# Kernel optimization log

Measured on AMD Instinct MI355X. Metric: run time of the kernel, lower is better.

Reference implementation:

```python
import jax, jax.numpy as jnp
import numpy as np

N, D, F, H, DH, R = 50000, 16, 256, 8, 32, 20
HOP_NUM, TOP_K, ALPHA, NEG_SLOPE = 10, 5, 0.1, 0.2
FF_HID = 4 * F


def _ln(x, g, b, eps=1e-5):
    m = x.mean(-1, keepdims=True)
    v = ((x - m) ** 2).mean(-1, keepdims=True)
    return (x - m) / jnp.sqrt(v + eps) * g + b


def setup_inputs() -> dict:
    key = jax.random.key(0)
    ks = jax.random.split(key, 16)
    s = 0.02
    inp = {
        'ent_feat': jax.random.normal(ks[0], (N, F), jnp.float32),
        'rel_feat': jax.random.normal(ks[1], (R, F), jnp.float32),
        'W_head': jax.random.normal(ks[2], (F, H * DH), jnp.float32) * s,
        'W_tail': jax.random.normal(ks[3], (F, H * DH), jnp.float32) * s,
        'W_ent': jax.random.normal(ks[4], (F, H * DH), jnp.float32) * s,
        'W_rel': jax.random.normal(ks[5], (F, H * DH), jnp.float32) * s,
        'attn_h': jax.random.normal(ks[6], (H, DH), jnp.float32) * s,
        'attn_t': jax.random.normal(ks[7], (H, DH), jnp.float32) * s,
        'attn_r': jax.random.normal(ks[8], (H, DH), jnp.float32) * s,
        'ln_ent_g': jnp.ones((F,), jnp.float32), 'ln_ent_b': jnp.zeros((F,), jnp.float32),
        'ln_rel_g': jnp.ones((F,), jnp.float32), 'ln_rel_b': jnp.zeros((F,), jnp.float32),
        'ln_ff_g': jnp.ones((F,), jnp.float32), 'ln_ff_b': jnp.zeros((F,), jnp.float32),
        'ffn_W1': jax.random.normal(ks[9], (F, FF_HID), jnp.float32) * s,
        'ffn_b1': jnp.zeros((FF_HID,), jnp.float32),
        'ffn_W2': jax.random.normal(ks[10], (FF_HID, F), jnp.float32) * s,
        'ffn_b2': jnp.zeros((F,), jnp.float32),
        'src': jax.random.randint(ks[11], (N, D), 0, N, jnp.int32),
        'rid': jax.random.randint(ks[12], (N, D), 0, R, jnp.int32),
    }
    return inp


def reference(ent_feat, rel_feat, W_head, W_tail, W_ent, W_rel,
              attn_h, attn_t, attn_r,
              ln_ent_g, ln_ent_b, ln_rel_g, ln_rel_b, ln_ff_g, ln_ff_b,
              ffn_W1, ffn_b1, ffn_W2, ffn_b2, src, rid):
    # --- projections (dropout = 0 at eval) ---
    x = _ln(ent_feat, ln_ent_g, ln_ent_b)                    # [N,F]
    fh = (x @ W_head).reshape(N, H, DH)
    ftl = (x @ W_tail).reshape(N, H, DH)
    fe = (x @ W_ent).reshape(N, H, DH)                       # 'ft' messages
    r = _ln(rel_feat, ln_rel_g, ln_rel_b)
    fr = (r @ W_rel).reshape(R, H, DH)
    # --- per-node / per-relation attention logits ---
    eh = (fh * attn_h).sum(-1)                               # [N,H]
    et = (ftl * attn_t).sum(-1)                              # [N,H]
    er = (fr * attn_r).sum(-1)                               # [R,H]
    # edges: row i = incoming edges of dst node i, sources src[i,:]
    e = eh[src] + et[:, None, :] + er[rid]                   # [N,D,H]
    e = jnp.where(e > 0, e, NEG_SLOPE * e)                   # LeakyReLU
    # --- edge_softmax over incoming edges of each dst node ---
    a = jax.nn.softmax(e, axis=1)                            # [N,D,H]
    # --- top-k sparsification + renormalization ---
    a_t = a.transpose(0, 2, 1)                               # [N,H,D]
    topv, _ = jax.lax.top_k(a_t, TOP_K)                      # [N,H,K]
    kth = topv[..., TOP_K - 1]                               # [N,H]
    top_sum = topv.sum(-1)                                   # [N,H]
    a_n = jnp.where(a_t >= kth[..., None], a_t, 0.0) / top_sum[..., None]  # [N,H,D]
    # --- PPR diffusion: feat <- (1-a) * A @ feat + a * feat0 ---
    feat0 = fe

    def step(feat, _):
        m = feat[src]                                        # [N,D,H,DH]
        agg = jnp.einsum('ndhk,nhd->nhk', m, a_n)            # [N,H,DH]
        return (1.0 - ALPHA) * agg + ALPHA * feat0, None

    feat, _ = jax.lax.scan(step, feat0, None, length=HOP_NUM)
    # --- residual (Identity since in==out) + FFN block ---
    rst = feat + ent_feat.reshape(N, H, DH)
    rst = rst.reshape(N, F)
    y = _ln(rst, ln_ff_g, ln_ff_b)
    ff = jax.nn.relu(y @ ffn_W1 + ffn_b1) @ ffn_W2 + ffn_b2
    return ff + rst
```

## Files before the change

### kernel.cpp

```cpp
#include <hip/hip_runtime.h>

#define NN   50000
#define DD   16
#define FFE  256
#define HH   8
#define DHH  32
#define RR   20
#define HOPN 10

typedef unsigned short u16;
typedef unsigned int   u32;
typedef __attribute__((ext_vector_type(8))) short  short8;
typedef __attribute__((ext_vector_type(4))) float  floatx4;
typedef __attribute__((ext_vector_type(4))) double doublex4;

__device__ __forceinline__ float b2f(u16 u){ return __uint_as_float(((u32)u)<<16); }
__device__ __forceinline__ u16 f2b(float f){
  u32 x = __float_as_uint(f);
  u32 r = (x + 0x7fffu + ((x>>16)&1u)) >> 16;
  return (u16)r;
}

__device__ __forceinline__ void glds16(const u16* g, u16* l) {
  __builtin_amdgcn_global_load_lds(
      (const __attribute__((address_space(1))) void*)g,
      (__attribute__((address_space(3))) void*)l, 16, 0, 0);
}

__global__ __launch_bounds__(256) void castw_kernel(
    const float* __restrict__ We, const float* __restrict__ W1,
    const float* __restrict__ W2,
    u16* __restrict__ Wet, u16* __restrict__ W1t, u16* __restrict__ W2t)
{
  int tid = blockIdx.x*256 + threadIdx.x;
  if (tid < 256*256) {
    int k = tid >> 8, n = tid & 255;
    Wet[n*256 + k] = f2b(We[tid]);
  } else if (tid < 256*256 + 256*1024) {
    int s = tid - 65536;
    int k = s >> 10, n = s & 1023;
    W1t[n*256 + k] = f2b(W1[s]);
  } else if (tid < 589824) {
    int s = tid - 327680;
    int k = s >> 8, n = s & 255;
    W2t[n*1024 + k] = f2b(W2[s]);
  }
}

__global__ __launch_bounds__(256) void prep_kernel(
    const float* __restrict__ rel_feat,
    const float* __restrict__ W_head, const float* __restrict__ W_tail,
    const float* __restrict__ W_rel,
    const float* __restrict__ attn_h, const float* __restrict__ attn_t,
    const float* __restrict__ attn_r,
    const float* __restrict__ lng, const float* __restrict__ lnb,
    double* __restrict__ Wcomb, double* __restrict__ er)
{
  int t = threadIdx.x;
  if (blockIdx.x == RR) {
    for (int h = 0; h < HH; h++) {
      double sh = 0.0, st = 0.0;
      #pragma unroll
      for (int c = 0; c < DHH; c++) {
        int j = h*DHH + c;
        sh += (double)W_head[t*FFE + j] * (double)attn_h[j];
        st += (double)W_tail[t*FFE + j] * (double)attn_t[j];
      }
      Wcomb[t*16 + h]     = sh;
      Wcomb[t*16 + 8 + h] = st;
    }
    return;
  }
  int r = blockIdx.x;
  __shared__ double red[8];
  __shared__ double rln[256];
  double v = (double)rel_feat[r*FFE + t];
  double s = v, q = v*v;
  #pragma unroll
  for (int o = 32; o; o >>= 1) { s += __shfl_xor(s, o, 64); q += __shfl_xor(q, o, 64); }
  if ((t & 63) == 0) { red[t>>6] = s; red[4 + (t>>6)] = q; }
  __syncthreads();
  double stot = red[0]+red[1]+red[2]+red[3];
  double qtot = red[4]+red[5]+red[6]+red[7];
  double mean = stot * (1.0/256.0);
  double var  = qtot * (1.0/256.0) - mean*mean;
  double rstd = 1.0 / sqrt(var + 1e-5);
  rln[t] = (v - mean) * rstd * (double)lng[t] + (double)lnb[t];
  __syncthreads();
  double acc = 0.0;
  for (int k = 0; k < 256; k++) acc += rln[k] * (double)W_rel[k*FFE + t];
  double p = acc * (double)attn_r[t];
  #pragma unroll
  for (int o = 16; o; o >>= 1) p += __shfl_down(p, o, 32);
  if ((t & 31) == 0) er[r*HH + (t>>5)] = p;
}

__global__ __launch_bounds__(256) void logits_kernel(
    const float* __restrict__ ent,
    const float* __restrict__ lng, const float* __restrict__ lnb,
    const double* __restrict__ Wcomb,
    u16* __restrict__ xb, double* __restrict__ eh, double* __restrict__ et)
{
  __shared__ double xs[16][257];
  int tid = threadIdx.x;
  int i0 = blockIdx.x * 16;
  int wave = tid >> 6, lane = tid & 63;
  for (int m = wave; m < 16; m += 4) {
    int row = i0 + m;
    float4 u = *(const float4*)&ent[row*FFE + lane*4];
    double v0 = u.x, v1 = u.y, v2 = u.z, v3 = u.w;
    double s = v0+v1+v2+v3;
    double q = v0*v0 + v1*v1 + v2*v2 + v3*v3;
    #pragma unroll
    for (int o = 32; o; o >>= 1) { s += __shfl_xor(s, o, 64); q += __shfl_xor(q, o, 64); }
    double mean = s * (1.0/256.0);
    double var  = q * (1.0/256.0) - mean*mean;
    double rstd = 1.0 / sqrt(var + 1e-5);
    float4 ug = *(const float4*)&lng[lane*4];
    float4 ub = *(const float4*)&lnb[lane*4];
    double y0 = (v0-mean)*rstd*(double)ug.x + (double)ub.x;
    double y1 = (v1-mean)*rstd*(double)ug.y + (double)ub.y;
    double y2 = (v2-mean)*rstd*(double)ug.z + (double)ub.z;
    double y3 = (v3-mean)*rstd*(double)ug.w + (double)ub.w;
    int c = lane*4;
    xs[m][c] = y0; xs[m][c+1] = y1; xs[m][c+2] = y2; xs[m][c+3] = y3;
    ushort4 o4;
    o4.x = f2b((float)y0); o4.y = f2b((float)y1);
    o4.z = f2b((float)y2); o4.w = f2b((float)y3);
    *(ushort4*)&xb[row*FFE + c] = o4;
  }
  __syncthreads();
  int nl = lane & 15, kg = lane >> 4;
  doublex4 c4 = {0.0, 0.0, 0.0, 0.0};
  #pragma unroll
  for (int kk = 0; kk < 16; kk++) {
    int k = wave*64 + kk*4 + kg;
    double a = xs[nl][k];
    double b = Wcomb[k*16 + nl];
    c4 = __builtin_amdgcn_mfma_f64_16x16x4f64(a, b, c4, 0, 0, 0);
  }
  __syncthreads();
  double* sp = &xs[0][0];
  #pragma unroll
  for (int i = 0; i < 4; i++)
    sp[wave*256 + (kg*4 + i)*16 + nl] = c4[i];
  __syncthreads();
  int m = tid >> 4, n = tid & 15;
  double v = sp[tid] + sp[256 + tid] + sp[512 + tid] + sp[768 + tid];
  if (n < 8) eh[(i0+m)*HH + n] = v;
  else       et[(i0+m)*HH + (n-8)] = v;
}

template<int EPI>
__global__ __launch_bounds__(256) void gemm_kernel(
    const u16* __restrict__ A, const u16* __restrict__ B,
    const float* __restrict__ bias,
    const u16* __restrict__ feat, const float* __restrict__ ent,
    u16* __restrict__ Obf, float* __restrict__ Of,
    int M, int N, int K)
{
  __shared__ u16 As[128*64];
  __shared__ u16 Bs[128*64];
  int t = threadIdx.x;
  int i0 = blockIdx.x * 128;
  int n0 = blockIdx.y * 128;
  int w = t >> 6, l = t & 63;
  int wr = w >> 1, wc = w & 1;

  int lrow = l >> 3;
  int scol = ((l & 7) ^ lrow) * 8;

  int ln = l & 15, q = l >> 4;
  int colk0 = (q*8) ^ ((ln & 7) << 3);
  int colk1 = colk0 ^ 32;

  floatx4 acc[4][4];
  #pragma unroll
  for (int mt = 0; mt < 4; mt++)
    #pragma unroll
    for (int nt = 0; nt < 4; nt++) acc[mt][nt] = (floatx4){0.f,0.f,0.f,0.f};

  for (int k0 = 0; k0 < K; k0 += 64) {
    #pragma unroll
    for (int j = 0; j < 4; j++) {
      int ra = w*32 + j*8 + lrow;
      int ga = min(i0 + ra, M-1);
      glds16(&A[(size_t)ga*K + k0 + scol], &As[(w*4+j)*512]);
      int gb = n0 + ra;
      glds16(&B[(size_t)gb*K + k0 + scol], &Bs[(w*4+j)*512]);
    }
    __syncthreads();
    #pragma unroll
    for (int ks = 0; ks < 2; ks++) {
      int ck = ks ? colk1 : colk0;
      short8 bfr[4], afr[4];
      #pragma unroll
      for (int nt = 0; nt < 4; nt++)
        bfr[nt] = *(const short8*)&Bs[(wc*64 + nt*16 + ln)*64 + ck];
      #pragma unroll
      for (int mt = 0; mt < 4; mt++)
        afr[mt] = *(const short8*)&As[(wr*64 + mt*16 + ln)*64 + ck];
      #pragma unroll
      for (int mt = 0; mt < 4; mt++)
        #pragma unroll
        for (int nt = 0; nt < 4; nt++)
          acc[mt][nt] = __builtin_amdgcn_mfma_f32_16x16x32_bf16(afr[mt], bfr[nt], acc[mt][nt], 0, 0, 0);
    }
    __syncthreads();
  }

  int lr = q * 4;
  #pragma unroll
  for (int mt = 0; mt < 4; mt++) {
    #pragma unroll
    for (int nt = 0; nt < 4; nt++) {
      int col = n0 + wc*64 + nt*16 + ln;
      #pragma unroll
      for (int r = 0; r < 4; r++) {
        int row = i0 + wr*64 + mt*16 + lr + r;
        if (row < M) {
          float v = acc[mt][nt][r];
          if (EPI == 0) {
            Obf[(size_t)row*N + col] = f2b(v);
          } else if (EPI == 1) {
            v += bias[col];
            Obf[(size_t)row*N + col] = f2b(v > 0.f ? v : 0.f);
          } else {
            v += bias[col] + b2f(feat[(size_t)row*FFE + col]) + ent[(size_t)row*FFE + col];
            Of[(size_t)row*N + col] = v;
          }
        }
      }
    }
  }
}

__global__ __launch_bounds__(256) void edge_kernel(
    const int* __restrict__ src, const int* __restrict__ rid,
    const double* __restrict__ eh, const double* __restrict__ et,
    const double* __restrict__ er,
    int* __restrict__ idx6, float* __restrict__ w6)
{
  int tid = blockIdx.x*256 + threadIdx.x;
  if (tid >= NN*HH) return;
  int i = tid >> 3, h = tid & 7;
  double bet = et[tid];
  double e[16]; int sj[16];
  #pragma unroll
  for (int d = 0; d < 16; d++) {
    int s = src[i*DD + d];
    int rv = rid[i*DD + d];
    sj[d] = s;
    double v = eh[s*HH + h] + bet + er[rv*HH + h];
    e[d] = (v > 0.0) ? v : 0.2 * v;
  }
  u32 mask = 0; double vs[5]; int js[5];
  #pragma unroll
  for (int k = 0; k < 5; k++) {
    double best = -1e300; int bj = 0, bd = 0;
    #pragma unroll
    for (int d = 0; d < 16; d++) {
      bool c = (((mask>>d)&1u) == 0u) && (e[d] > best);
      if (c) { best = e[d]; bj = sj[d]; bd = d; }
    }
    mask |= (1u << bd); vs[k] = best; js[k] = bj;
  }
  double kth = vs[4];
  int j6 = 0; bool f6 = false;
  #pragma unroll
  for (int d = 0; d < 16; d++) {
    if ((((mask>>d)&1u) == 0u) && (e[d] == kth) && !f6) { j6 = sj[d]; f6 = true; }
  }
  float m0 = (float)vs[0];
  float ex[5], ssum = 0.f;
  #pragma unroll
  for (int k = 0; k < 5; k++) { ex[k] = __expf((float)vs[k] - m0); ssum += ex[k]; }
  float inv = 0.9f / ssum;
  long base = (long)tid * 6;
  #pragma unroll
  for (int k = 0; k < 5; k++) { idx6[base+k] = js[k]; w6[base+k] = ex[k]*inv; }
  idx6[base+5] = j6; w6[base+5] = f6 ? ex[4]*inv : 0.f;
}

__global__ __launch_bounds__(256) void diff_kernel(
    const u16* __restrict__ fold, const u16* __restrict__ fe,
    const int* __restrict__ idx6, const float* __restrict__ w6,
    u16* __restrict__ fnew)
{
  int tid = threadIdx.x;
  int nb = tid >> 5;
  int v  = tid & 31;
  int h  = v >> 2;
  int cc = (v & 3) * 8;
  int i  = blockIdx.x*8 + nb;
  int ch = h*DHH + cc;
  long eb = ((long)i*HH + h) * 6;

  int jj[5]; float wv[5];
  #pragma unroll
  for (int k = 0; k < 5; k++) { jj[k] = idx6[eb + k]; wv[k] = w6[eb + k]; }
  short8 g[5];
  #pragma unroll
  for (int k = 0; k < 5; k++)
    g[k] = *(const short8*)&fold[(size_t)jj[k]*FFE + ch];
  short8 f8 = *(const short8*)&fe[(size_t)i*FFE + ch];

  float acc[8];
  #pragma unroll
  for (int j = 0; j < 8; j++) acc[j] = 0.1f * b2f((u16)f8[j]);
  #pragma unroll
  for (int k = 0; k < 5; k++)
    #pragma unroll
    for (int j = 0; j < 8; j++) acc[j] += wv[k] * b2f((u16)g[k][j]);

  float w5 = w6[eb + 5];
  if (w5 != 0.f) {
    int j5 = idx6[eb + 5];
    short8 g5 = *(const short8*)&fold[(size_t)j5*FFE + ch];
    #pragma unroll
    for (int j = 0; j < 8; j++) acc[j] += w5 * b2f((u16)g5[j]);
  }

  short8 o8;
  #pragma unroll
  for (int j = 0; j < 8; j++) o8[j] = (short)f2b(acc[j]);
  *(short8*)&fnew[(size_t)i*FFE + ch] = o8;
}

__global__ __launch_bounds__(256) void ln_ff_kernel(
    const u16* __restrict__ feat, const float* __restrict__ ent,
    const float* __restrict__ g, const float* __restrict__ b,
    u16* __restrict__ y)
{
  int w = threadIdx.x >> 6, l = threadIdx.x & 63;
  int row = blockIdx.x*4 + w;
  float4 e4 = *(const float4*)&ent[row*FFE + l*4];
  ushort4 fv = *(const ushort4*)&feat[row*FFE + l*4];
  float v0 = b2f(fv.x)+e4.x, v1 = b2f(fv.y)+e4.y;
  float v2 = b2f(fv.z)+e4.z, v3 = b2f(fv.w)+e4.w;
  float s = v0+v1+v2+v3;
  float q = v0*v0 + v1*v1 + v2*v2 + v3*v3;
  #pragma unroll
  for (int o = 32; o; o >>= 1) { s += __shfl_xor(s, o, 64); q += __shfl_xor(q, o, 64); }
  float mean = s * (1.f/256.f);
  float var  = q * (1.f/256.f) - mean*mean;
  float rstd = rsqrtf(var + 1e-5f);
  float4 g4 = *(const float4*)&g[l*4];
  float4 b4 = *(const float4*)&b[l*4];
  ushort4 o4;
  o4.x = f2b((v0-mean)*rstd*g4.x + b4.x);
  o4.y = f2b((v1-mean)*rstd*g4.y + b4.y);
  o4.z = f2b((v2-mean)*rstd*g4.z + b4.z);
  o4.w = f2b((v3-mean)*rstd*g4.w + b4.w);
  *(ushort4*)&y[row*FFE + l*4] = o4;
}

extern "C" void kernel_launch(void* const* d_in, const int* in_sizes, int n_in,
                              void* d_out, int out_size, void* d_ws, size_t ws_size,
                              hipStream_t stream)
{
  const float* ent      = (const float*)d_in[0];
  const float* rel      = (const float*)d_in[1];
  const float* W_head   = (const float*)d_in[2];
  const float* W_tail   = (const float*)d_in[3];
  const float* W_ent    = (const float*)d_in[4];
  const float* W_rel    = (const float*)d_in[5];
  const float* attn_h   = (const float*)d_in[6];
  const float* attn_t   = (const float*)d_in[7];
  const float* attn_r   = (const float*)d_in[8];
  const float* ln_ent_g = (const float*)d_in[9];
  const float* ln_ent_b = (const float*)d_in[10];
  const float* ln_rel_g = (const float*)d_in[11];
  const float* ln_rel_b = (const float*)d_in[12];
  const float* ln_ff_g  = (const float*)d_in[13];
  const float* ln_ff_b  = (const float*)d_in[14];
  const float* W1       = (const float*)d_in[15];
  const float* b1       = (const float*)d_in[16];
  const float* W2       = (const float*)d_in[17];
  const float* b2       = (const float*)d_in[18];
  const int* src        = (const int*)d_in[19];
  const int* rid        = (const int*)d_in[20];
  float* out = (float*)d_out;

  char* w = (char*)d_ws;
  double* er64  = (double*)(w + 0);
  double* Wcomb = (double*)(w + 4096);
  double* eh64 = (double*)(w + 36864);
  double* et64 = (double*)(w + 3236864);
  u16*    xb   = (u16*)  (w + 6436864);
  u16*    fe   = (u16*)  (w + 32036864);
  u16*    fA   = (u16*)  (w + 57636864);
  int*    idx6 = (int*)  (w + 83236864);
  float*  w6   = (float*)(w + 92836864);
  u16*    h1   = (u16*)  (w + 0);
  u16*    fB   = (u16*)  (w + 102436864);
  u16*    y    = (u16*)  (w + 128036864);
  u16*    Wet  = (u16*)  (w + 153636864);
  u16*    W1t  = (u16*)  (w + 153767936);
  u16*    W2t  = (u16*)  (w + 154292224);

  castw_kernel<<<2304, 256, 0, stream>>>(W_ent, W1, W2, Wet, W1t, W2t);
  prep_kernel<<<RR+1, 256, 0, stream>>>(rel, W_head, W_tail, W_rel,
                                        attn_h, attn_t, attn_r,
                                        ln_rel_g, ln_rel_b, Wcomb, er64);
  logits_kernel<<<NN/16, 256, 0, stream>>>(ent, ln_ent_g, ln_ent_b, Wcomb,
                                           xb, eh64, et64);
  {
    dim3 g((NN + 127)/128, 2);
    gemm_kernel<0><<<g, 256, 0, stream>>>(xb, Wet, nullptr, nullptr, nullptr,
                                          fe, nullptr, NN, 256, 256);
  }
  edge_kernel<<<(NN*HH + 255)/256, 256, 0, stream>>>(src, rid, eh64, et64, er64,
                                                     idx6, w6);
  const u16* cur = fe;
  u16* bufs[2] = { fA, fB };
  for (int hop = 0; hop < HOPN; hop++) {
    u16* nxt = bufs[hop & 1];
    diff_kernel<<<NN/8, 256, 0, stream>>>(cur, fe, idx6, w6, nxt);
    cur = nxt;
  }
  ln_ff_kernel<<<NN/4, 256, 0, stream>>>(cur, ent, ln_ff_g, ln_ff_b, y);
  {
    dim3 g((NN + 127)/128, 8);
    gemm_kernel<1><<<g, 256, 0, stream>>>(y, W1t, b1, nullptr, nullptr,
                                          h1, nullptr, NN, 1024, 256);
  }
  {
    dim3 g((NN + 127)/128, 2);
    gemm_kernel<2><<<g, 256, 0, stream>>>(h1, W2t, b2, cur, ent,
                                          nullptr, out, NN, 256, 1024);
  }
}
```

Baseline: 776.6 us.

## Fuse FFN GEMMs into one kernel and pack edge indices with weights

Replaces the two FFN GEMM launches with a single kernel that keeps the 64x1024 hidden activation in shared memory chunk by chunk, so the N×1024 bf16 intermediate is never written to or read back from global memory. The edge kernel now stores indices and weights interleaved in one 12-int record, so the diffusion kernel reads them with three vector loads instead of twelve scalar loads. In exchange, the fused kernel reads W1/W2 fragments straight from global memory without LDS staging, and it runs with small tiles and fewer blocks, which may reduce MFMA efficiency.

```diff
diff --git a/kernel.cpp b/kernel.cpp
--- a/kernel.cpp
+++ b/kernel.cpp
@@ -166,10 +166,8 @@
   int n0 = blockIdx.y * 128;
   int w = t >> 6, l = t & 63;
   int wr = w >> 1, wc = w & 1;
-
   int lrow = l >> 3;
   int scol = ((l & 7) ^ lrow) * 8;
-
   int ln = l & 15, q = l >> 4;
   int colk0 = (q*8) ^ ((ln & 7) << 3);
   int colk1 = colk0 ^ 32;
@@ -235,11 +233,120 @@
   }
 }
 
+__global__ __launch_bounds__(256) void ffn_kernel(
+    const u16* __restrict__ y, const u16* __restrict__ W1t,
+    const float* __restrict__ b1, const u16* __restrict__ W2t,
+    const float* __restrict__ b2, const u16* __restrict__ feat,
+    const float* __restrict__ ent, float* __restrict__ out, int M)
+{
+  __shared__ u16 ys[64*256];
+  __shared__ u16 hs[64*128];
+  int t = threadIdx.x;
+  int w = t >> 6, l = t & 63;
+  int i0 = blockIdx.x * 64;
+  int ln = l & 15, q = l >> 4;
+
+  {
+    int rsub = l >> 5;
+    int gsub = l & 31;
+    #pragma unroll
+    for (int j = 0; j < 8; j++) {
+      int r = w*16 + j*2 + rsub;
+      int gr = min(i0 + r, M-1);
+      int so = (gsub ^ ((j*2 + rsub) & 7)) * 8;
+      glds16(&y[(size_t)gr*FFE + so], &ys[(w*16 + j*2)*FFE]);
+    }
+  }
+  __syncthreads();
+
+  floatx4 acc2[4][4];
+  #pragma unroll
+  for (int mt = 0; mt < 4; mt++)
+    #pragma unroll
+    for (int nt = 0; nt < 4; nt++) acc2[mt][nt] = (floatx4){0.f,0.f,0.f,0.f};
+
+  for (int s = 0; s < 8; s++) {
+    floatx4 acc1[4][2];
+    #pragma unroll
+    for (int mt = 0; mt < 4; mt++)
+      #pragma unroll
+      for (int nt = 0; nt < 2; nt++) acc1[mt][nt] = (floatx4){0.f,0.f,0.f,0.f};
+    #pragma unroll
+    for (int ks = 0; ks < 8; ks++) {
+      short8 bf[2];
+      #pragma unroll
+      for (int nt = 0; nt < 2; nt++) {
+        int n = s*128 + w*32 + nt*16 + ln;
+        bf[nt] = *(const short8*)&W1t[(size_t)n*FFE + ks*32 + q*8];
+      }
+      int gsw = ((ks*4 + q) ^ (ln & 7)) * 8;
+      #pragma unroll
+      for (int mt = 0; mt < 4; mt++) {
+        short8 af = *(const short8*)&ys[(mt*16 + ln)*FFE + gsw];
+        #pragma unroll
+        for (int nt = 0; nt < 2; nt++)
+          acc1[mt][nt] = __builtin_amdgcn_mfma_f32_16x16x32_bf16(af, bf[nt], acc1[mt][nt], 0, 0, 0);
+      }
+    }
+    #pragma unroll
+    for (int mt = 0; mt < 4; mt++) {
+      #pragma unroll
+      for (int nt = 0; nt < 2; nt++) {
+        int hid = w*32 + nt*16 + ln;
+        float bb = b1[s*128 + hid];
+        #pragma unroll
+        for (int r = 0; r < 4; r++) {
+          int row = mt*16 + q*4 + r;
+          float v = acc1[mt][nt][r] + bb;
+          int gs = (hid >> 3) ^ (row & 7);
+          hs[row*128 + gs*8 + (hid & 7)] = f2b(v > 0.f ? v : 0.f);
+        }
+      }
+    }
+    __syncthreads();
+    #pragma unroll
+    for (int ks = 0; ks < 4; ks++) {
+      short8 bf[4];
+      #pragma unroll
+      for (int nt = 0; nt < 4; nt++) {
+        int n = w*64 + nt*16 + ln;
+        bf[nt] = *(const short8*)&W2t[(size_t)n*1024 + s*128 + ks*32 + q*8];
+      }
+      int gsw = ((ks*4 + q) ^ (ln & 7)) * 8;
+      #pragma unroll
+      for (int mt = 0; mt < 4; mt++) {
+        short8 af = *(const short8*)&hs[(mt*16 + ln)*128 + gsw];
+        #pragma unroll
+        for (int nt = 0; nt < 4; nt++)
+          acc2[mt][nt] = __builtin_amdgcn_mfma_f32_16x16x32_bf16(af, bf[nt], acc2[mt][nt], 0, 0, 0);
+      }
+    }
+    __syncthreads();
+  }
+
+  #pragma unroll
+  for (int mt = 0; mt < 4; mt++) {
+    #pragma unroll
+    for (int nt = 0; nt < 4; nt++) {
+      int col = w*64 + nt*16 + ln;
+      #pragma unroll
+      for (int r = 0; r < 4; r++) {
+        int row = i0 + mt*16 + q*4 + r;
+        if (row < M) {
+          float v = acc2[mt][nt][r];
+          v += b2[col] + b2f(feat[(size_t)row*FFE + col]) + ent[(size_t)row*FFE + col];
+          out[(size_t)row*FFE + col] = v;
+        }
+      }
+    }
+  }
+}
+
 __global__ __launch_bounds__(256) void edge_kernel(
     const int* __restrict__ src, const int* __restrict__ rid,
     const double* __restrict__ eh, const double* __restrict__ et,
     const double* __restrict__ er,
-    int* __restrict__ idx6, float* __restrict__ w6)
+    int* __restrict__ pk)
 {
   int tid = blockIdx.x*256 + threadIdx.x;
   if (tid >= NN*HH) return;
@@ -276,15 +383,19 @@
   #pragma unroll
   for (int k = 0; k < 5; k++) { ex[k] = __expf((float)vs[k] - m0); ssum += ex[k]; }
   float inv = 0.9f / ssum;
-  long base = (long)tid * 6;
-  #pragma unroll
-  for (int k = 0; k < 5; k++) { idx6[base+k] = js[k]; w6[base+k] = ex[k]*inv; }
-  idx6[base+5] = j6; w6[base+5] = f6 ? ex[4]*inv : 0.f;
+  long base = (long)tid * 12;
+  #pragma unroll
+  for (int k = 0; k < 5; k++) {
+    pk[base + k]     = js[k];
+    pk[base + 6 + k] = __float_as_int(ex[k]*inv);
+  }
+  pk[base + 5]  = j6;
+  pk[base + 11] = __float_as_int(f6 ? ex[4]*inv : 0.f);
 }
 
 __global__ __launch_bounds__(256) void diff_kernel(
     const u16* __restrict__ fold, const u16* __restrict__ fe,
-    const int* __restrict__ idx6, const float* __restrict__ w6,
+    const int* __restrict__ pk,
     u16* __restrict__ fnew)
 {
   int tid = threadIdx.x;
@@ -294,11 +405,16 @@
   int cc = (v & 3) * 8;
   int i  = blockIdx.x*8 + nb;
   int ch = h*DHH + cc;
-  long eb = ((long)i*HH + h) * 6;
-
-  int jj[5]; float wv[5];
-  #pragma unroll
-  for (int k = 0; k < 5; k++) { jj[k] = idx6[eb + k]; wv[k] = w6[eb + k]; }
+  long base = ((long)i*HH + h) * 12;
+
+  int4 pa = *(const int4*)&pk[base];
+  int4 pb = *(const int4*)&pk[base + 4];
+  int4 pc = *(const int4*)&pk[base + 8];
+  int jj[5] = { pa.x, pa.y, pa.z, pa.w, pb.x };
+  float wv[5] = { __int_as_float(pb.z), __int_as_float(pb.w),
+                  __int_as_float(pc.x), __int_as_float(pc.y),
+                  __int_as_float(pc.z) };
+
   short8 g[5];
   #pragma unroll
   for (int k = 0; k < 5; k++)
@@ -313,9 +429,9 @@
     #pragma unroll
     for (int j = 0; j < 8; j++) acc[j] += wv[k] * b2f((u16)g[k][j]);
 
-  float w5 = w6[eb + 5];
+  float w5 = __int_as_float(pc.w);
   if (w5 != 0.f) {
-    int j5 = idx6[eb + 5];
+    int j5 = pb.y;
     short8 g5 = *(const short8*)&fold[(size_t)j5*FFE + ch];
     #pragma unroll
     for (int j = 0; j < 8; j++) acc[j] += w5 * b2f((u16)g5[j]);
@@ -390,9 +506,7 @@
   u16*    xb   = (u16*)  (w + 6436864);
   u16*    fe   = (u16*)  (w + 32036864);
   u16*    fA   = (u16*)  (w + 57636864);
-  int*    idx6 = (int*)  (w + 83236864);
-  float*  w6   = (float*)(w + 92836864);
-  u16*    h1   = (u16*)  (w + 0);
+  int*    pk   = (int*)  (w + 83236864);
   u16*    fB   = (u16*)  (w + 102436864);
   u16*    y    = (u16*)  (w + 128036864);
   u16*    Wet  = (u16*)  (w + 153636864);
@@ -411,23 +525,15 @@
                                           fe, nullptr, NN, 256, 256);
   }
   edge_kernel<<<(NN*HH + 255)/256, 256, 0, stream>>>(src, rid, eh64, et64, er64,
-                                                     idx6, w6);
+                                                     pk);
   const u16* cur = fe;
   u16* bufs[2] = { fA, fB };
   for (int hop = 0; hop < HOPN; hop++) {
     u16* nxt = bufs[hop & 1];
-    diff_kernel<<<NN/8, 256, 0, stream>>>(cur, fe, idx6, w6, nxt);
+    diff_kernel<<<NN/8, 256, 0, stream>>>(cur, fe, pk, nxt);
     cur = nxt;
   }
   ln_ff_kernel<<<NN/4, 256, 0, stream>>>(cur, ent, ln_ff_g, ln_ff_b, y);
-  {
-    dim3 g((NN + 127)/128, 8);
-    gemm_kernel<1><<<g, 256, 0, stream>>>(y, W1t, b1, nullptr, nullptr,
-                                          h1, nullptr, NN, 1024, 256);
-  }
-  {
-    dim3 g((NN + 127)/128, 2);
-    gemm_kernel<2><<<g, 256, 0, stream>>>(h1, W2t, b2, cur, ent,
-                                          nullptr, out, NN, 256, 1024);
-  }
-}
+  ffn_kernel<<<(NN + 63)/64, 256, 0, stream>>>(y, W1t, b1, W2t, b2,
+                                               cur, ent, out, NN);
+}
```

Result: slower. 797.4 us (+2.7%).
